# Kernel tuning notes

Hardware: AMD Instinct MI355X
Metric: run time of the kernel (lower is better)

Reference implementation:

```python
import jax, jax.numpy as jnp
import numpy as np

MAX_AGENTS = 64
IN_DIM = 256
HID_DIM = 512
OUT_DIM = 256
MAX_CHILDREN = 8
BATCH = 1024


def setup_inputs() -> dict:
    key = jax.random.key(0)
    k1, k2, k3, k4, k5 = jax.random.split(key, 5)
    W1 = jax.random.normal(k1, (MAX_AGENTS, IN_DIM, HID_DIM), dtype=jnp.float32) * 0.02
    b1 = jnp.zeros((MAX_AGENTS, HID_DIM), dtype=jnp.float32)
    W2 = jax.random.normal(k2, (MAX_AGENTS, HID_DIM, OUT_DIM), dtype=jnp.float32) * 0.02
    b2 = jnp.zeros((MAX_AGENTS, OUT_DIM), dtype=jnp.float32)
    router_weights = jax.random.normal(k3, (MAX_AGENTS, HID_DIM, MAX_CHILDREN), dtype=jnp.float32) * 0.01
    agent_indices = jax.random.randint(k4, (BATCH,), 0, MAX_AGENTS, dtype=jnp.int64 if jax.config.jax_enable_x64 else jnp.int32)
    x = jax.random.normal(k5, (BATCH, IN_DIM), dtype=jnp.float32)
    return {
        "x": x,
        "W1": W1,
        "b1": b1,
        "W2": W2,
        "b2": b2,
        "router_weights": router_weights,
        "agent_indices": agent_indices,
    }


def reference(x, W1, b1, W2, b2, router_weights, agent_indices):
    # Gather per-sample weights (same as torch advanced indexing W1[agent_indices])
    w1 = W1[agent_indices]           # [B, In, Hid]
    b1g = b1[agent_indices]          # [B, Hid]
    w2 = W2[agent_indices]           # [B, Hid, Out]
    b2g = b2[agent_indices]          # [B, Out]
    rw = router_weights[agent_indices]  # [B, Hid, C]

    # per-sample MLP: bmm with a singleton row -> einsum
    h = jax.nn.relu(jnp.einsum('bi,bih->bh', x, w1) + b1g)      # [B, Hid]
    out = jnp.einsum('bh,bho->bo', h, w2) + b2g                 # [B, Out]
    r_logits = jnp.einsum('bh,bhc->bc', h, rw)                  # [B, C]
    return (h, out, r_logits)
```

## Files before the change

kernel.cpp:

```cpp
#include <hip/hip_runtime.h>

#define IN_DIM   256
#define HID_DIM  512
#define OUT_DIM  256
#define N_CHILD  8
#define BATCH    1024

#define SB    16
#define XPAD  20
#define MAXCH 128

extern "C" __global__ __launch_bounds__(1024)
void prep_sort(const int* __restrict__ raw, int* __restrict__ sorted,
               int* __restrict__ ch_agent, int* __restrict__ ch_start,
               int* __restrict__ ch_len, float* __restrict__ zdst)
{
    const int t = threadIdx.x;
    if (blockIdx.x > 0) {
        const int total4 = (BATCH * (OUT_DIM + N_CHILD)) / 4;
        const float4 z = make_float4(0.f, 0.f, 0.f, 0.f);
        for (int i = (blockIdx.x - 1) * 1024 + t; i < total4; i += 4 * 1024)
            ((float4*)zdst)[i] = z;
        return;
    }
    __shared__ int cnt[64], cnt2[64], start[64];
    __shared__ int is32, totch;
    if (t < 64) { cnt[t] = 0; cnt2[t] = 0; }
    if (t == 0) is32 = 0;
    __syncthreads();
    if (raw[2 * (t & 511) + 1] != 0) is32 = 1;
    __syncthreads();
    const int a = (is32 ? raw[t] : raw[2 * t]) & 63;
    atomicAdd(&cnt[a], 1);
    __syncthreads();
    if (t < 64) {
        const int c   = cnt[t];
        const int nch = (c + SB - 1) / SB;
        int sc = c, sn = nch;
        #pragma unroll
        for (int d = 1; d < 64; d <<= 1) {
            const int vc = __shfl_up(sc, d);
            const int vn = __shfl_up(sn, d);
            if (t >= d) { sc += vc; sn += vn; }
        }
        const int off = sc - c;
        start[t] = off;
        const int chb = sn - nch;
        for (int p = 0, j = 0; p < c; p += SB, ++j) {
            ch_agent[chb + j] = t;
            ch_start[chb + j] = off + p;
            ch_len[chb + j]   = (c - p < SB) ? (c - p) : SB;
        }
        if (t == 63) totch = sn;
    }
    __syncthreads();
    if (t >= totch && t < MAXCH) ch_len[t] = 0;
    const int pos = start[a] + atomicAdd(&cnt2[a], 1);
    sorted[pos] = t;
}

extern "C" __global__ __launch_bounds__(256)
void k1_mlp1(const float* __restrict__ x, const float* __restrict__ W1,
             const float* __restrict__ b1, const float* __restrict__ rw,
             const int* __restrict__ sorted, const int* __restrict__ ch_agent,
             const int* __restrict__ ch_start, const int* __restrict__ ch_len,
             float* __restrict__ h_out, float* __restrict__ r_out)
{
    const int chunk = blockIdx.x;
    const int len = ch_len[chunk];
    if (len == 0) return;
    const int a  = ch_agent[chunk];
    const int cs = ch_start[chunk];
    const int t  = threadIdx.x;
    const int bcol = blockIdx.y * 64;

    __shared__ float xT[IN_DIM * XPAD];
    __shared__ float wS[64 * 64];
    __shared__ int   sid[SB];

    if (t < SB) sid[t] = sorted[cs + (t < len ? t : len - 1)];
    __syncthreads();

    #pragma unroll
    for (int s = 0; s < SB; ++s)
        xT[t * XPAD + s] = x[(size_t)sid[s] * IN_DIM + t];

    const float* Wb = W1 + (size_t)a * IN_DIM * HID_DIM + bcol;
    const int cg = t & 15;
    const int kq = (t >> 4) & 3;
    const int w  = t >> 6;
    const bool act = (w * 4) < len;

    float acc[16];
    #pragma unroll
    for (int i = 0; i < 16; ++i) acc[i] = 0.f;

    for (int p = 0; p < IN_DIM / 64; ++p) {
        __syncthreads();
        #pragma unroll
        for (int i = 0; i < 4; ++i) {
            const int id  = t + i * 256;
            const int row = id >> 4;
            const int c4  = (id & 15) * 4;
            *(float4*)(&wS[row * 64 + c4]) =
                *(const float4*)(Wb + (size_t)(p * 64 + row) * HID_DIM + c4);
        }
        __syncthreads();
        if (act) {
            #pragma unroll
            for (int i = 0; i < 16; ++i) {
                const int row = i * 4 + kq;
                const float4 wv = *(const float4*)(&wS[row * 64 + cg * 4]);
                const float4 xv = *(const float4*)(&xT[(p * 64 + row) * XPAD + w * 4]);
                const float wa[4] = {wv.x, wv.y, wv.z, wv.w};
                const float xa[4] = {xv.x, xv.y, xv.z, xv.w};
                #pragma unroll
                for (int c = 0; c < 4; ++c)
                    #pragma unroll
                    for (int s = 0; s < 4; ++s)
                        acc[c * 4 + s] = fmaf(wa[c], xa[s], acc[c * 4 + s]);
            }
        }
    }

    if (!act) return;

    #pragma unroll
    for (int i = 0; i < 16; ++i) {
        acc[i] += __shfl_xor(acc[i], 16);
        acc[i] += __shfl_xor(acc[i], 32);
    }

    if (kq != 0) return;

    const float4 bv = *(const float4*)(b1 + a * HID_DIM + bcol + cg * 4);
    const float ba[4] = {bv.x, bv.y, bv.z, bv.w};
    float hv[16];
    #pragma unroll
    for (int c = 0; c < 4; ++c)
        #pragma unroll
        for (int s = 0; s < 4; ++s)
            hv[c * 4 + s] = fmaxf(acc[c * 4 + s] + ba[c], 0.f);

    #pragma unroll
    for (int s = 0; s < 4; ++s) {
        float4 v = make_float4(hv[0 * 4 + s], hv[1 * 4 + s],
                               hv[2 * 4 + s], hv[3 * 4 + s]);
        *(float4*)(h_out + (size_t)sid[w * 4 + s] * HID_DIM + bcol + cg * 4) = v;
    }

    float rp[32];
    #pragma unroll
    for (int i = 0; i < 32; ++i) rp[i] = 0.f;
    const float* rwa = rw + (size_t)a * HID_DIM * N_CHILD
                          + (size_t)(bcol + cg * 4) * N_CHILD;
    #pragma unroll
    for (int j = 0; j < 4; ++j)
        #pragma unroll
        for (int ch = 0; ch < 8; ++ch) {
            const float rv = rwa[j * N_CHILD + ch];
            #pragma unroll
            for (int s = 0; s < 4; ++s)
                rp[s * 8 + ch] = fmaf(hv[j * 4 + s], rv, rp[s * 8 + ch]);
        }
    #pragma unroll
    for (int i = 0; i < 32; ++i) {
        rp[i] += __shfl_xor(rp[i], 1);
        rp[i] += __shfl_xor(rp[i], 2);
        rp[i] += __shfl_xor(rp[i], 4);
        rp[i] += __shfl_xor(rp[i], 8);
    }
    if (cg == 0) {
        #pragma unroll
        for (int s = 0; s < 4; ++s) {
            const int sg = w * 4 + s;
            if (sg < len) {
                float* rdst = r_out + (size_t)sid[sg] * N_CHILD;
                #pragma unroll
                for (int ch = 0; ch < 8; ++ch)
                    atomicAdd(rdst + ch, rp[s * 8 + ch]);
            }
        }
    }
}

extern "C" __global__ __launch_bounds__(256)
void k2_mlp2(const float* __restrict__ h, const float* __restrict__ W2,
             const float* __restrict__ b2,
             const int* __restrict__ sorted, const int* __restrict__ ch_agent,
             const int* __restrict__ ch_start, const int* __restrict__ ch_len,
             float* __restrict__ o_out)
{
    const int chunk = blockIdx.x;
    const int len = ch_len[chunk];
    if (len == 0) return;
    const int a  = ch_agent[chunk];
    const int cs = ch_start[chunk];
    const int t  = threadIdx.x;
    const int bcol = blockIdx.y * 64;
    const int kb   = blockIdx.z * 256;

    __shared__ float hT[64 * XPAD];
    __shared__ float wS[64 * 64];
    __shared__ int   sid[SB];

    if (t < SB) sid[t] = sorted[cs + (t < len ? t : len - 1)];
    __syncthreads();

    const float* Wb = W2 + (size_t)a * HID_DIM * OUT_DIM + bcol;
    const int cg = t & 15;
    const int kq = (t >> 4) & 3;
    const int w  = t >> 6;
    const bool act = (w * 4) < len;

    float acc[16];
    #pragma unroll
    for (int i = 0; i < 16; ++i) acc[i] = 0.f;

    for (int p = 0; p < 4; ++p) {
        const int k0 = kb + p * 64;
        __syncthreads();
        {
            const int row = t & 63;
            const int sb  = (t >> 6) * 4;
            #pragma unroll
            for (int j = 0; j < 4; ++j)
                hT[row * XPAD + sb + j] =
                    h[(size_t)sid[sb + j] * HID_DIM + k0 + row];
        }
        #pragma unroll
        for (int i = 0; i < 4; ++i) {
            const int id  = t + i * 256;
            const int r2  = id >> 4;
            const int c4  = (id & 15) * 4;
            *(float4*)(&wS[r2 * 64 + c4]) =
                *(const float4*)(Wb + (size_t)(k0 + r2) * OUT_DIM + c4);
        }
        __syncthreads();
        if (act) {
            #pragma unroll
            for (int i = 0; i < 16; ++i) {
                const int row = i * 4 + kq;
                const float4 wv = *(const float4*)(&wS[row * 64 + cg * 4]);
                const float4 xv = *(const float4*)(&hT[row * XPAD + w * 4]);
                const float wa[4] = {wv.x, wv.y, wv.z, wv.w};
                const float xa[4] = {xv.x, xv.y, xv.z, xv.w};
                #pragma unroll
                for (int c = 0; c < 4; ++c)
                    #pragma unroll
                    for (int s = 0; s < 4; ++s)
                        acc[c * 4 + s] = fmaf(wa[c], xa[s], acc[c * 4 + s]);
            }
        }
    }

    if (!act) return;
    #pragma unroll
    for (int i = 0; i < 16; ++i) {
        acc[i] += __shfl_xor(acc[i], 16);
        acc[i] += __shfl_xor(acc[i], 32);
    }
    if (kq == 0) {
        float4 bv = make_float4(0.f, 0.f, 0.f, 0.f);
        if (blockIdx.z == 0)
            bv = *(const float4*)(b2 + a * OUT_DIM + bcol + cg * 4);
        #pragma unroll
        for (int s = 0; s < 4; ++s) {
            const int g = w * 4 + s;
            if (g < len) {
                float* op = o_out + (size_t)sid[g] * OUT_DIM + bcol + cg * 4;
                atomicAdd(op + 0, acc[0 * 4 + s] + bv.x);
                atomicAdd(op + 1, acc[1 * 4 + s] + bv.y);
                atomicAdd(op + 2, acc[2 * 4 + s] + bv.z);
                atomicAdd(op + 3, acc[3 * 4 + s] + bv.w);
            }
        }
    }
}

extern "C" void kernel_launch(void* const* d_in, const int* in_sizes, int n_in,
                              void* d_out, int out_size, void* d_ws, size_t ws_size,
                              hipStream_t stream) {
    const float* x  = (const float*)d_in[0];
    const float* W1 = (const float*)d_in[1];
    const float* b1 = (const float*)d_in[2];
    const float* W2 = (const float*)d_in[3];
    const float* b2 = (const float*)d_in[4];
    const float* rw = (const float*)d_in[5];
    const int* raw  = (const int*)d_in[6];

    int* ws       = (int*)d_ws;
    int* sorted   = ws;
    int* ch_agent = ws + 1024;
    int* ch_start = ws + 1152;
    int* ch_len   = ws + 1280;

    float* out   = (float*)d_out;
    float* h_out = out;
    float* o_out = h_out + (size_t)BATCH * HID_DIM;
    float* r_out = o_out + (size_t)BATCH * OUT_DIM;

    hipLaunchKernelGGL(prep_sort, dim3(5), dim3(1024), 0, stream,
                       raw, sorted, ch_agent, ch_start, ch_len, o_out);
    hipLaunchKernelGGL(k1_mlp1, dim3(MAXCH, 8), dim3(256), 0, stream,
                       x, W1, b1, rw, sorted, ch_agent, ch_start, ch_len,
                       h_out, r_out);
    hipLaunchKernelGGL(k2_mlp2, dim3(MAXCH, 4, 2), dim3(256), 0, stream,
                       h_out, W2, b2, sorted, ch_agent, ch_start, ch_len, o_out);
}
```

Measured before the change: 133.5 us.

## Register-prefetch weight tiles and drop split-K atomics in second MLP

Both MLP kernels now load the next 64-row weight tile (and, in k2, the next h slice) into registers while the current tile is being consumed, so global-load latency overlaps the FMA loop. k2 no longer splits the K dimension across blockIdx.z. Each block covers the full hidden dimension and writes its output with plain float4 stores instead of atomicAdds. Because of that, the output no longer needs zeroing, and prep_sort only clears the router-logit region. The trade-off is half as many k2 blocks, each with a longer serial K loop, and higher register pressure from the prefetch buffers.

```diff
diff --git a/kernel.cpp b/kernel.cpp
--- a/kernel.cpp
+++ b/kernel.cpp
@@ -17,9 +17,9 @@
 {
     const int t = threadIdx.x;
     if (blockIdx.x > 0) {
-        const int total4 = (BATCH * (OUT_DIM + N_CHILD)) / 4;
+        const int total4 = (BATCH * N_CHILD) / 4;
         const float4 z = make_float4(0.f, 0.f, 0.f, 0.f);
-        for (int i = (blockIdx.x - 1) * 1024 + t; i < total4; i += 4 * 1024)
+        for (int i = t; i < total4; i += 1024)
             ((float4*)zdst)[i] = z;
         return;
     }
@@ -81,11 +81,17 @@
     if (t < SB) sid[t] = sorted[cs + (t < len ? t : len - 1)];
     __syncthreads();
 
+    const float* Wb = W1 + (size_t)a * IN_DIM * HID_DIM + bcol;
+    const int sr  = t >> 4;
+    const int sc4 = (t & 15) * 4;
+    #define WLD(P,I) (*(const float4*)(Wb + (size_t)((P)*64 + sr + (I)*16) * HID_DIM + sc4))
+
+    float4 wr0 = WLD(0,0), wr1 = WLD(0,1), wr2 = WLD(0,2), wr3 = WLD(0,3);
+
     #pragma unroll
     for (int s = 0; s < SB; ++s)
         xT[t * XPAD + s] = x[(size_t)sid[s] * IN_DIM + t];
 
-    const float* Wb = W1 + (size_t)a * IN_DIM * HID_DIM + bcol;
     const int cg = t & 15;
     const int kq = (t >> 4) & 3;
     const int w  = t >> 6;
@@ -97,15 +103,15 @@
 
     for (int p = 0; p < IN_DIM / 64; ++p) {
         __syncthreads();
-        #pragma unroll
-        for (int i = 0; i < 4; ++i) {
-            const int id  = t + i * 256;
-            const int row = id >> 4;
-            const int c4  = (id & 15) * 4;
-            *(float4*)(&wS[row * 64 + c4]) =
-                *(const float4*)(Wb + (size_t)(p * 64 + row) * HID_DIM + c4);
-        }
+        *(float4*)(&wS[(sr +  0) * 64 + sc4]) = wr0;
+        *(float4*)(&wS[(sr + 16) * 64 + sc4]) = wr1;
+        *(float4*)(&wS[(sr + 32) * 64 + sc4]) = wr2;
+        *(float4*)(&wS[(sr + 48) * 64 + sc4]) = wr3;
         __syncthreads();
+        if (p < 3) {
+            wr0 = WLD(p+1,0); wr1 = WLD(p+1,1);
+            wr2 = WLD(p+1,2); wr3 = WLD(p+1,3);
+        }
         if (act) {
             #pragma unroll
             for (int i = 0; i < 16; ++i) {
@@ -122,6 +128,7 @@
             }
         }
     }
+    #undef WLD
 
     if (!act) return;
 
@@ -198,7 +205,6 @@
     const int cs = ch_start[chunk];
     const int t  = threadIdx.x;
     const int bcol = blockIdx.y * 64;
-    const int kb   = blockIdx.z * 256;
 
     __shared__ float hT[64 * XPAD];
     __shared__ float wS[64 * 64];
@@ -208,6 +214,16 @@
     __syncthreads();
 
     const float* Wb = W2 + (size_t)a * HID_DIM * OUT_DIM + bcol;
+    const int sr   = t >> 4;
+    const int sc4  = (t & 15) * 4;
+    const int hrow = t & 63;
+    const int hsb  = (t >> 6) * 4;
+    #define WLD2(P,I) (*(const float4*)(Wb + (size_t)((P)*64 + sr + (I)*16) * OUT_DIM + sc4))
+    #define HLD(P,J)  (h[(size_t)sid[hsb + (J)] * HID_DIM + (P)*64 + hrow])
+
+    float4 wr0 = WLD2(0,0), wr1 = WLD2(0,1), wr2 = WLD2(0,2), wr3 = WLD2(0,3);
+    float  hr0 = HLD(0,0),  hr1 = HLD(0,1),  hr2 = HLD(0,2),  hr3 = HLD(0,3);
+
     const int cg = t & 15;
     const int kq = (t >> 4) & 3;
     const int w  = t >> 6;
@@ -217,26 +233,23 @@
     #pragma unroll
     for (int i = 0; i < 16; ++i) acc[i] = 0.f;
 
-    for (int p = 0; p < 4; ++p) {
-        const int k0 = kb + p * 64;
+    for (int p = 0; p < HID_DIM / 64; ++p) {
         __syncthreads();
-        {
-            const int row = t & 63;
-            const int sb  = (t >> 6) * 4;
-            #pragma unroll
-            for (int j = 0; j < 4; ++j)
-                hT[row * XPAD + sb + j] =
-                    h[(size_t)sid[sb + j] * HID_DIM + k0 + row];
-        }
-        #pragma unroll
-        for (int i = 0; i < 4; ++i) {
-            const int id  = t + i * 256;
-            const int r2  = id >> 4;
-            const int c4  = (id & 15) * 4;
-            *(float4*)(&wS[r2 * 64 + c4]) =
-                *(const float4*)(Wb + (size_t)(k0 + r2) * OUT_DIM + c4);
-        }
+        hT[hrow * XPAD + hsb + 0] = hr0;
+        hT[hrow * XPAD + hsb + 1] = hr1;
+        hT[hrow * XPAD + hsb + 2] = hr2;
+        hT[hrow * XPAD + hsb + 3] = hr3;
+        *(float4*)(&wS[(sr +  0) * 64 + sc4]) = wr0;
+        *(float4*)(&wS[(sr + 16) * 64 + sc4]) = wr1;
+        *(float4*)(&wS[(sr + 32) * 64 + sc4]) = wr2;
+        *(float4*)(&wS[(sr + 48) * 64 + sc4]) = wr3;
         __syncthreads();
+        if (p < 7) {
+            wr0 = WLD2(p+1,0); wr1 = WLD2(p+1,1);
+            wr2 = WLD2(p+1,2); wr3 = WLD2(p+1,3);
+            hr0 = HLD(p+1,0);  hr1 = HLD(p+1,1);
+            hr2 = HLD(p+1,2);  hr3 = HLD(p+1,3);
+        }
         if (act) {
             #pragma unroll
             for (int i = 0; i < 16; ++i) {
@@ -253,6 +266,8 @@
             }
         }
     }
+    #undef WLD2
+    #undef HLD
 
     if (!act) return;
     #pragma unroll
@@ -261,18 +276,16 @@
         acc[i] += __shfl_xor(acc[i], 32);
     }
     if (kq == 0) {
-        float4 bv = make_float4(0.f, 0.f, 0.f, 0.f);
-        if (blockIdx.z == 0)
-            bv = *(const float4*)(b2 + a * OUT_DIM + bcol + cg * 4);
+        const float4 bv = *(const float4*)(b2 + a * OUT_DIM + bcol + cg * 4);
         #pragma unroll
         for (int s = 0; s < 4; ++s) {
             const int g = w * 4 + s;
             if (g < len) {
-                float* op = o_out + (size_t)sid[g] * OUT_DIM + bcol + cg * 4;
-                atomicAdd(op + 0, acc[0 * 4 + s] + bv.x);
-                atomicAdd(op + 1, acc[1 * 4 + s] + bv.y);
-                atomicAdd(op + 2, acc[2 * 4 + s] + bv.z);
-                atomicAdd(op + 3, acc[3 * 4 + s] + bv.w);
+                float4 v = make_float4(acc[0 * 4 + s] + bv.x,
+                                       acc[1 * 4 + s] + bv.y,
+                                       acc[2 * 4 + s] + bv.z,
+                                       acc[3 * 4 + s] + bv.w);
+                *(float4*)(o_out + (size_t)sid[g] * OUT_DIM + bcol + cg * 4) = v;
             }
         }
     }
@@ -300,11 +313,11 @@
     float* o_out = h_out + (size_t)BATCH * HID_DIM;
     float* r_out = o_out + (size_t)BATCH * OUT_DIM;
 
-    hipLaunchKernelGGL(prep_sort, dim3(5), dim3(1024), 0, stream,
-                       raw, sorted, ch_agent, ch_start, ch_len, o_out);
+    hipLaunchKernelGGL(prep_sort, dim3(2), dim3(1024), 0, stream,
+                       raw, sorted, ch_agent, ch_start, ch_len, r_out);
     hipLaunchKernelGGL(k1_mlp1, dim3(MAXCH, 8), dim3(256), 0, stream,
                        x, W1, b1, rw, sorted, ch_agent, ch_start, ch_len,
                        h_out, r_out);
-    hipLaunchKernelGGL(k2_mlp2, dim3(MAXCH, 4, 2), dim3(256), 0, stream,
+    hipLaunchKernelGGL(k2_mlp2, dim3(MAXCH, 4), dim3(256), 0, stream,
                        h_out, W2, b2, sorted, ch_agent, ch_start, ch_len, o_out);
 }
```

New measurement: 130.9 us. About the same (-1.9%).
